# Kernel tuning notes

Measured on AMD Instinct MI355X. Metric: run time of the kernel, lower is better.

The kernel has to match this reference:

```python
import jax, jax.numpy as jnp
import numpy as np

HIDDEN = 256
NUM_REL = 6
NUM_BASES = 30
N_NODES = 50000
N_EDGES = 800000


def rgcn_gate_layer(x, src, dst, etype, basis, att, root, bias, gate_w, gate_b):
    # Basis-decomposed relation weights: W_r = sum_b att[r,b] * basis[b]
    N = x.shape[0]
    W = jnp.einsum('rb,bio->rio', att, basis)           # [R, d, d]
    # Transform all nodes under every relation (cheaper than per-edge matmul
    # since N*R < E), then gather the per-edge message.
    xw = jnp.einsum('nd,rde->rne', x, W)                # [R, N, d]
    msg = xw[etype, src]                                # [E, d]
    # Scalar sigmoid gate per edge message
    g = jax.nn.sigmoid(msg @ gate_w + gate_b)           # [E, 1]
    gated = g * msg
    # Mean aggregation over incoming edges per destination node
    agg = jax.ops.segment_sum(gated, dst, num_segments=N)
    deg = jax.ops.segment_sum(jnp.ones((src.shape[0], 1), x.dtype), dst,
                              num_segments=N)
    agg = agg / jnp.maximum(deg, 1.0)
    return agg + x @ root + bias


def setup_inputs() -> dict:
    key = jax.random.key(0)
    ks = jax.random.split(key, 16)
    d = HIDDEN
    inp = {
        'x': jax.random.normal(ks[0], (N_NODES, d), jnp.float32),
        'edge_src': jax.random.randint(ks[1], (N_EDGES,), 0, N_NODES, jnp.int32),
        'edge_dst': jax.random.randint(ks[2], (N_EDGES,), 0, N_NODES, jnp.int32),
        'edge_type': jax.random.randint(ks[3], (N_EDGES,), 0, NUM_REL, jnp.int32),
    }
    def glorot(k, shape):
        fan = shape[-2] + shape[-1]
        return jax.random.uniform(k, shape, jnp.float32,
                                  -np.sqrt(6.0 / fan), np.sqrt(6.0 / fan))
    for li, off in ((1, 4), (2, 10)):
        inp[f'basis{li}'] = glorot(ks[off + 0], (NUM_BASES, d, d))
        inp[f'att{li}'] = glorot(ks[off + 1], (NUM_REL, NUM_BASES))
        inp[f'root{li}'] = glorot(ks[off + 2], (d, d))
        inp[f'bias{li}'] = jnp.zeros((d,), jnp.float32)
        inp[f'gate_w{li}'] = glorot(ks[off + 3], (d, 1))
        inp[f'gate_b{li}'] = jnp.zeros((1,), jnp.float32)
    return inp


def reference(x, edge_src, edge_dst, edge_type,
              basis1, att1, root1, bias1, gate_w1, gate_b1,
              basis2, att2, root2, bias2, gate_w2, gate_b2):
    h = jax.nn.relu(rgcn_gate_layer(x, edge_src, edge_dst, edge_type,
                                    basis1, att1, root1, bias1,
                                    gate_w1, gate_b1))
    out = rgcn_gate_layer(h, edge_src, edge_dst, edge_type,
                          basis2, att2, root2, bias2, gate_w2, gate_b2)
    return out
```

## Files before the change

kernel.cpp:

```cpp
#include <hip/hip_runtime.h>
#include <cmath>

#define HIDDEN 256
#define NUM_REL 6
#define KA 1536
#define KB 1792
#define NKSTEP 28
#define KASTEP 24
#define CTSTRIDE 28672

typedef float f32x4_t __attribute__((ext_vector_type(4)));
typedef short bf16x8_t __attribute__((ext_vector_type(8)));

__device__ __forceinline__ float bf2f(ushort u) {
  return __uint_as_float(((uint)u) << 16);
}
__device__ __forceinline__ ushort f2bf(float f) {
  uint u = __float_as_uint(f);
  u += 0x7FFFu + ((u >> 16) & 1u);
  return (ushort)(u >> 16);
}

__global__ void compute_W_kernel(const float* __restrict__ att,
                                 const float* __restrict__ basis,
                                 float* __restrict__ Wall) {
  int idx = blockIdx.x * blockDim.x + threadIdx.x;
  int r  = idx >> 16;
  int io = idx & 65535;
  float s = 0.f;
#pragma unroll
  for (int b = 0; b < 30; ++b)
    s += att[r * 30 + b] * basis[(size_t)b * 65536 + io];
  Wall[idx] = s;
}

__global__ __launch_bounds__(256) void gatevec_kernel(
    const float* __restrict__ Wall, const float* __restrict__ gw,
    float* __restrict__ gatevec) {
  const int wave = (blockIdx.x * blockDim.x + threadIdx.x) >> 6;
  const int l = threadIdx.x & 63;
  const int r = wave >> 8, d = wave & 255;
  float4 wv = ((const float4*)(Wall + (size_t)r * 65536 + d * 256))[l];
  float4 gv = ((const float4*)gw)[l];
  float dot = wv.x * gv.x + wv.y * gv.y + wv.z * gv.z + wv.w * gv.w;
#pragma unroll
  for (int off = 32; off; off >>= 1) dot += __shfl_xor(dot, off);
  if (l == 0) gatevec[r * 256 + d] = dot;
}

__global__ void build_BTf(const float* __restrict__ Wall,
                          const float* __restrict__ root,
                          ushort* __restrict__ BTf) {
  int tid = blockIdx.x * blockDim.x + threadIdx.x;
  if (tid >= KB * 256) return;
  int o = tid & 255, gk = tid >> 8;
  int r = gk >> 8, kin = gk & 255;
  float v = (r < 6) ? Wall[(size_t)r * 65536 + kin * 256 + o]
                    : root[(size_t)kin * 256 + o];
  size_t idx = (size_t)(o >> 4) * CTSTRIDE + (size_t)(gk >> 3) * 128 +
               (o & 15) * 8 + (gk & 7);
  BTf[idx] = f2bf(v);
}

__global__ void cvt_f32_bf16(const float* __restrict__ in,
                             ushort* __restrict__ out, int n4) {
  int i = blockIdx.x * blockDim.x + threadIdx.x;
  if (i >= n4) return;
  float4 v = ((const float4*)in)[i];
  ushort4 o;
  o.x = f2bf(v.x); o.y = f2bf(v.y); o.z = f2bf(v.z); o.w = f2bf(v.w);
  ((ushort4*)out)[i] = o;
}

__global__ __launch_bounds__(256) void gdot_kernel(
    const ushort* __restrict__ xb, const float* __restrict__ gatevec,
    const float* __restrict__ gate_b, float* __restrict__ G, int N) {
  const int wave = (blockIdx.x * blockDim.x + threadIdx.x) >> 6;
  if (wave >= N) return;
  const int l = threadIdx.x & 63;
  ushort4 xv = ((const ushort4*)(xb + (size_t)wave * 256))[l];
  const float x0 = bf2f(xv.x), x1 = bf2f(xv.y), x2 = bf2f(xv.z), x3 = bf2f(xv.w);
  float out = 0.f;
#pragma unroll
  for (int r = 0; r < NUM_REL; ++r) {
    float4 gv = ((const float4*)(gatevec + r * 256))[l];
    float d = x0 * gv.x + x1 * gv.y + x2 * gv.z + x3 * gv.w;
#pragma unroll
    for (int off = 32; off; off >>= 1) d += __shfl_xor(d, off);
    if (l == r) out = d;
  }
  if (l < NUM_REL) {
    const float gb = gate_b[0];
    G[(size_t)l * N + wave] = 1.f / (1.f + __expf(-(out + gb)));
  }
}

#define ACCUM(rj, gj, vj)                                                  \
  do {                                                                    \
    const float fx = (gj)*bf2f((vj).x), fy = (gj)*bf2f((vj).y);           \
    const float fz = (gj)*bf2f((vj).z), fw = (gj)*bf2f((vj).w);           \
    switch (rj) {                                                         \
      case 0: a0x += fx; a0y += fy; a0z += fz; a0w += fw; break;          \
      case 1: a1x += fx; a1y += fy; a1z += fz; a1w += fw; break;          \
      case 2: a2x += fx; a2y += fy; a2z += fz; a2w += fw; break;          \
      case 3: a3x += fx; a3y += fy; a3z += fz; a3w += fw; break;          \
      case 4: a4x += fx; a4y += fy; a4z += fz; a4w += fw; break;          \
      default: a5x += fx; a5y += fy; a5z += fz; a5w += fw; break;         \
    }                                                                     \
  } while (0)

#define RELOF(ei) ((ei >= b1) + (ei >= b2) + (ei >= b3) + (ei >= b4) + (ei >= b5))

__global__ __launch_bounds__(256) void edge_agg(
    const ushort* __restrict__ xb, const float* __restrict__ G,
    const int* __restrict__ rp8, const int* __restrict__ src_s,
    ushort* __restrict__ A, int N) {
  const int n = (blockIdx.x * blockDim.x + threadIdx.x) >> 6;
  if (n >= N) return;
  const int l = threadIdx.x & 63;
  const int b0 = rp8[n * 8 + 0], b1 = rp8[n * 8 + 1], b2 = rp8[n * 8 + 2];
  const int b3 = rp8[n * 8 + 3], b4 = rp8[n * 8 + 4], b5 = rp8[n * 8 + 5];
  const int b6 = rp8[n * 8 + 6];

  float a0x = 0, a0y = 0, a0z = 0, a0w = 0, a1x = 0, a1y = 0, a1z = 0, a1w = 0;
  float a2x = 0, a2y = 0, a2z = 0, a2w = 0, a3x = 0, a3y = 0, a3z = 0, a3w = 0;
  float a4x = 0, a4y = 0, a4z = 0, a4w = 0, a5x = 0, a5y = 0, a5z = 0, a5w = 0;

  int e = b0;
  for (; e + 7 < b6; e += 8) {
    const int s0 = src_s[e + 0], s1 = src_s[e + 1];
    const int s2 = src_s[e + 2], s3 = src_s[e + 3];
    const int s4 = src_s[e + 4], s5 = src_s[e + 5];
    const int s6 = src_s[e + 6], s7 = src_s[e + 7];
    const ushort4 v0 = ((const ushort4*)(xb + (size_t)s0 * 256))[l];
    const ushort4 v1 = ((const ushort4*)(xb + (size_t)s1 * 256))[l];
    const ushort4 v2 = ((const ushort4*)(xb + (size_t)s2 * 256))[l];
    const ushort4 v3 = ((const ushort4*)(xb + (size_t)s3 * 256))[l];
    const ushort4 v4 = ((const ushort4*)(xb + (size_t)s4 * 256))[l];
    const ushort4 v5 = ((const ushort4*)(xb + (size_t)s5 * 256))[l];
    const ushort4 v6 = ((const ushort4*)(xb + (size_t)s6 * 256))[l];
    const ushort4 v7 = ((const ushort4*)(xb + (size_t)s7 * 256))[l];
    const int r0 = RELOF(e + 0), r1 = RELOF(e + 1), r2 = RELOF(e + 2),
              r3 = RELOF(e + 3), r4 = RELOF(e + 4), r5 = RELOF(e + 5),
              r6 = RELOF(e + 6), r7 = RELOF(e + 7);
    const float g0 = G[(size_t)r0 * N + s0], g1 = G[(size_t)r1 * N + s1];
    const float g2 = G[(size_t)r2 * N + s2], g3 = G[(size_t)r3 * N + s3];
    const float g4 = G[(size_t)r4 * N + s4], g5 = G[(size_t)r5 * N + s5];
    const float g6 = G[(size_t)r6 * N + s6], g7 = G[(size_t)r7 * N + s7];
    ACCUM(r0, g0, v0); ACCUM(r1, g1, v1); ACCUM(r2, g2, v2); ACCUM(r3, g3, v3);
    ACCUM(r4, g4, v4); ACCUM(r5, g5, v5); ACCUM(r6, g6, v6); ACCUM(r7, g7, v7);
  }
  for (; e < b6; ++e) {
    const int s0 = src_s[e];
    const ushort4 v0 = ((const ushort4*)(xb + (size_t)s0 * 256))[l];
    const int r0 = RELOF(e);
    const float g0 = G[(size_t)r0 * N + s0];
    ACCUM(r0, g0, v0);
  }

  const float inv = 1.f / fmaxf((float)(b6 - b0), 1.f);
  ushort* Arow = A + (size_t)n * KA;
  ushort4 o;
  o.x = f2bf(a0x * inv); o.y = f2bf(a0y * inv); o.z = f2bf(a0z * inv); o.w = f2bf(a0w * inv);
  ((ushort4*)(Arow + 0 * 256))[l] = o;
  o.x = f2bf(a1x * inv); o.y = f2bf(a1y * inv); o.z = f2bf(a1z * inv); o.w = f2bf(a1w * inv);
  ((ushort4*)(Arow + 1 * 256))[l] = o;
  o.x = f2bf(a2x * inv); o.y = f2bf(a2y * inv); o.z = f2bf(a2z * inv); o.w = f2bf(a2w * inv);
  ((ushort4*)(Arow + 2 * 256))[l] = o;
  o.x = f2bf(a3x * inv); o.y = f2bf(a3y * inv); o.z = f2bf(a3z * inv); o.w = f2bf(a3w * inv);
  ((ushort4*)(Arow + 3 * 256))[l] = o;
  o.x = f2bf(a4x * inv); o.y = f2bf(a4y * inv); o.z = f2bf(a4z * inv); o.w = f2bf(a4w * inv);
  ((ushort4*)(Arow + 4 * 256))[l] = o;
  o.x = f2bf(a5x * inv); o.y = f2bf(a5y * inv); o.z = f2bf(a5z * inv); o.w = f2bf(a5w * inv);
  ((ushort4*)(Arow + 5 * 256))[l] = o;
}

__global__ __launch_bounds__(256) void gemm_fused(const ushort* __restrict__ A,
                                                  const ushort* __restrict__ xb,
                                                  const ushort* __restrict__ BTf,
                                                  const float* __restrict__ bias,
                                                  void* __restrict__ outPtr,
                                                  int M, int mode) {
  __shared__ ushort As[3 * 8192];
  const int mB = (M + 127) >> 7;
  const int bid = blockIdx.x;
  const int yb = (bid >> 4) * 8 + (bid & 7);
  if (yb >= mB) return;
  const int colh = (bid >> 3) & 1;
  const int row0 = yb * 128;

  const int tid = threadIdx.x;
  const int w = tid >> 6, l = tid & 63;
  const int wm = w & 1, wn = w >> 1;

  const int srow = l >> 3;
  const int schunk = (l & 7) ^ srow;

  const ushort* Bbase = BTf + (size_t)(colh * 8 + wn * 4) * CTSTRIDE +
                        (l >> 4) * 128 + (l & 15) * 8;

  f32x4_t acc[4][4] = {};

  auto stage = [&](int k, int buf) {
    const int ko = k * 64;
#pragma unroll
    for (int i = 0; i < 4; ++i) {
      const int br = (w * 4 + i) * 8;
      const int ga = min(row0 + br + srow, M - 1);
      const ushort* gp = (k < KASTEP)
          ? (A + (size_t)ga * KA + ko + schunk * 8)
          : (xb + (size_t)ga * 256 + (ko - KA) + schunk * 8);
      __builtin_amdgcn_global_load_lds(
          (const __attribute__((address_space(1))) void*)gp,
          (__attribute__((address_space(3))) void*)(As + buf * 8192 + br * 64),
          16, 0, 0);
    }
  };

  bf16x8_t bc[2][4], bn[2][4];

  stage(0, 0);
  stage(1, 1);
#pragma unroll
  for (int kk = 0; kk < 2; ++kk)
#pragma unroll
    for (int n = 0; n < 4; ++n)
      bc[kk][n] = *(const bf16x8_t*)(Bbase + (size_t)n * CTSTRIDE + kk * 512);

#pragma unroll 2
  for (int k = 0; k < NKSTEP; ++k) {
    const int cur = k % 3;
    asm volatile("s_waitcnt vmcnt(12)" ::: "memory");
    __builtin_amdgcn_s_barrier();
#pragma unroll
    for (int kk = 0; kk < 2; ++kk)
#pragma unroll
      for (int n = 0; n < 4; ++n)
        bn[kk][n] = *(const bf16x8_t*)(Bbase + (size_t)n * CTSTRIDE +
                                       (size_t)(k + 1) * 1024 + kk * 512);
    __builtin_amdgcn_sched_barrier(0);
    if (k + 2 < NKSTEP) stage(k + 2, (k + 2) % 3);

#pragma unroll
    for (int kk = 0; kk < 2; ++kk) {
      const int swc = (kk * 4 + (l >> 4)) ^ (l & 7);
      bf16x8_t a[4];
#pragma unroll
      for (int m = 0; m < 4; ++m) {
        const int rr = wm * 64 + m * 16 + (l & 15);
        a[m] = *(const bf16x8_t*)(As + cur * 8192 + rr * 64 + swc * 8);
      }
#pragma unroll
      for (int m = 0; m < 4; ++m)
#pragma unroll
        for (int n = 0; n < 4; ++n)
          acc[m][n] = __builtin_amdgcn_mfma_f32_16x16x32_bf16(
              a[m], bc[kk][n], acc[m][n], 0, 0, 0);
    }
#pragma unroll
    for (int kk = 0; kk < 2; ++kk)
#pragma unroll
      for (int n = 0; n < 4; ++n)
        bc[kk][n] = bn[kk][n];
  }

  const int rbase = row0 + wm * 64 + (l >> 4) * 4;
  const int cbase = colh * 128 + wn * 64 + (l & 15);
#pragma unroll
  for (int n = 0; n < 4; ++n) {
    const int col = cbase + n * 16;
    const float bv = bias[col];
#pragma unroll
    for (int m = 0; m < 4; ++m)
#pragma unroll
      for (int i = 0; i < 4; ++i) {
        const int row = rbase + m * 16 + i;
        if (row < M) {
          float v = acc[m][n][i] + bv;
          if (mode == 0) {
            v = fmaxf(v, 0.f);
            ((ushort*)outPtr)[(size_t)row * 256 + col] = f2bf(v);
          } else {
            ((float*)outPtr)[(size_t)row * 256 + col] = v;
          }
        }
      }
  }
}

__global__ void hist_kernel(const int* __restrict__ dst,
                            const int* __restrict__ ety,
                            int* __restrict__ cnt, int E) {
  int stride = gridDim.x * blockDim.x;
  for (int e = blockIdx.x * blockDim.x + threadIdx.x; e < E; e += stride)
    atomicAdd(&cnt[dst[e] * 8 + ety[e]], 1);
}

__global__ void scan_reduce(const int* __restrict__ cnt,
                            int* __restrict__ blockSums, int n) {
  __shared__ int sd[256];
  int base = blockIdx.x * 1024;
  int t = threadIdx.x;
  int s = 0;
#pragma unroll
  for (int i = 0; i < 4; ++i) {
    int idx = base + t * 4 + i;
    s += (idx < n) ? cnt[idx] : 0;
  }
  sd[t] = s; __syncthreads();
  for (int off = 128; off; off >>= 1) {
    if (t < off) sd[t] += sd[t + off];
    __syncthreads();
  }
  if (t == 0) blockSums[blockIdx.x] = sd[0];
}

__global__ void scan_offsets(int* __restrict__ blockSums, int nb) {
  __shared__ int sd[512];
  const int t = threadIdx.x;
  const int v = (t < nb) ? blockSums[t] : 0;
  sd[t] = v; __syncthreads();
  for (int off = 1; off < 512; off <<= 1) {
    int u = (t >= off) ? sd[t - off] : 0;
    __syncthreads();
    sd[t] += u;
    __syncthreads();
  }
  if (t < nb) blockSums[t] = sd[t] - v;
}

__global__ void scan_write(const int* __restrict__ cnt,
                           const int* __restrict__ blockSums,
                           int* __restrict__ row_ptr, int n) {
  __shared__ int sd[256];
  int base = blockIdx.x * 1024;
  int t = threadIdx.x;
  int v[4]; int s = 0;
#pragma unroll
  for (int i = 0; i < 4; ++i) {
    int idx = base + t * 4 + i;
    v[i] = (idx < n) ? cnt[idx] : 0;
    s += v[i];
  }
  sd[t] = s; __syncthreads();
  for (int off = 1; off < 256; off <<= 1) {
    int val = (t >= off) ? sd[t - off] : 0;
    __syncthreads();
    sd[t] += val;
    __syncthreads();
  }
  int excl = blockSums[blockIdx.x] + sd[t] - s;
  for (int i = 0; i < 4; ++i) {
    int idx = base + t * 4 + i;
    if (idx < n) {
      row_ptr[idx] = excl;
      excl += v[i];
      if (idx == n - 1) row_ptr[n] = excl;
    }
  }
}

__global__ void scatter_kernel(const int* __restrict__ src,
                               const int* __restrict__ dst,
                               const int* __restrict__ ety,
                               int* __restrict__ cursor,
                               int* __restrict__ src_s, int E) {
  int stride = gridDim.x * blockDim.x;
  for (int e = blockIdx.x * blockDim.x + threadIdx.x; e < E; e += stride) {
    int bin = dst[e] * 8 + ety[e];
    int pos = atomicAdd(&cursor[bin], 1);
    src_s[pos] = src[e];
  }
}

static inline size_t align16(size_t x) { return (x + 15) & ~(size_t)15; }

extern "C" void kernel_launch(void* const* d_in, const int* in_sizes, int n_in,
                              void* d_out, int out_size, void* d_ws,
                              size_t ws_size, hipStream_t stream) {
  const float* x    = (const float*)d_in[0];
  const int*   src  = (const int*)d_in[1];
  const int*   dst  = (const int*)d_in[2];
  const int*   ety  = (const int*)d_in[3];

  const int N   = in_sizes[0] / HIDDEN;
  const int E   = in_sizes[1];
  const int RN2 = N * 8;

  char* p = (char*)d_ws;
  float* Wall    = (float*)p;  p += align16((size_t)NUM_REL * 65536 * 4);
  ushort* BTf    = (ushort*)p; p += align16(((size_t)16 * CTSTRIDE + 1024) * 2);
  float* gatevec = (float*)p;  p += align16((size_t)NUM_REL * 256 * 4);
  float* G       = (float*)p;  p += align16((size_t)NUM_REL * N * 4);
  ushort* xb0    = (ushort*)p; p += align16((size_t)N * HIDDEN * 2);
  ushort* xb1    = (ushort*)p; p += align16((size_t)N * HIDDEN * 2);
  int* cnt       = (int*)p;    p += align16((size_t)RN2 * 4);
  int* cursor    = (int*)p;    p += align16((size_t)RN2 * 4);
  int* row_ptr   = (int*)p;    p += align16((size_t)(RN2 + 1) * 4);
  int* blockSums = (int*)p;    p += 2048;
  int* src_s     = (int*)p;    p += align16((size_t)E * 4);
  ushort* A      = (ushort*)p;

  const int scanBlocks = (RN2 + 1023) / 1024;

  hipMemsetAsync(cnt, 0, (size_t)RN2 * sizeof(int), stream);
  hist_kernel<<<2048, 256, 0, stream>>>(dst, ety, cnt, E);
  scan_reduce<<<scanBlocks, 256, 0, stream>>>(cnt, blockSums, RN2);
  scan_offsets<<<1, 512, 0, stream>>>(blockSums, scanBlocks);
  scan_write<<<scanBlocks, 256, 0, stream>>>(cnt, blockSums, row_ptr, RN2);
  hipMemcpyAsync(cursor, row_ptr, (size_t)RN2 * sizeof(int),
                 hipMemcpyDeviceToDevice, stream);
  scatter_kernel<<<2048, 256, 0, stream>>>(src, dst, ety, cursor, src_s, E);

  cvt_f32_bf16<<<(N * 64 + 255) / 256, 256, 0, stream>>>(x, xb0, N * 64);

  const int nodeBlocks = (N * 64 + 255) / 256;
  const int mBlocks = (N + 127) / 128;
  const int gemmGrid = ((mBlocks + 7) / 8) * 16;

  for (int layer = 0; layer < 2; ++layer) {
    const float* bas  = (const float*)d_in[layer ? 10 : 4];
    const float* att  = (const float*)d_in[layer ? 11 : 5];
    const float* root = (const float*)d_in[layer ? 12 : 6];
    const float* bias = (const float*)d_in[layer ? 13 : 7];
    const float* gw   = (const float*)d_in[layer ? 14 : 8];
    const float* gb   = (const float*)d_in[layer ? 15 : 9];
    const ushort* xb  = layer ? xb1 : xb0;
    void* outp = layer ? d_out : (void*)xb1;
    const int mode = layer ? 1 : 0;

    compute_W_kernel<<<NUM_REL * 65536 / 256, 256, 0, stream>>>(att, bas, Wall);
    gatevec_kernel<<<384, 256, 0, stream>>>(Wall, gw, gatevec);
    build_BTf<<<(KB * 256 + 255) / 256, 256, 0, stream>>>(Wall, root, BTf);
    gdot_kernel<<<nodeBlocks, 256, 0, stream>>>(xb, gatevec, gb, G, N);
    edge_agg<<<nodeBlocks, 256, 0, stream>>>(xb, G, row_ptr, src_s, A, N);
    gemm_fused<<<gemmGrid, 256, 0, stream>>>(A, xb, BTf, bias, outp, N, mode);
  }
}
```

Measured before the change: 542.8 us.

## Fuse weight prep kernels, fold bf16 convert into gdot, retile GEMM to 64x256

Merges compute_W, gatevec and build_BTf into one prep_weights kernel that never materialises the fp32 W buffer. Folds the initial fp32-to-bf16 conversion of x into gdot_kernel and writes the cursor copy inside scan_write, removing a memcpy and a kernel launch. The GEMM changes from 128x128 tiles with 64-wide K steps to 64-row tiles spanning all 256 output columns with 32-wide K steps. Each block now reads its A rows once instead of twice, but it does half the MFMA work per K step and synchronises more often.

```diff
diff --git a/kernel.cpp b/kernel.cpp
--- a/kernel.cpp
+++ b/kernel.cpp
@@ -5,8 +5,8 @@
 #define NUM_REL 6
 #define KA 1536
 #define KB 1792
-#define NKSTEP 28
-#define KASTEP 24
+#define NK 56
+#define NKA 48
 #define CTSTRIDE 28672
 
 typedef float f32x4_t __attribute__((ext_vector_type(4)));
@@ -21,65 +21,53 @@
   return (ushort)(u >> 16);
 }
 
-__global__ void compute_W_kernel(const float* __restrict__ att,
-                                 const float* __restrict__ basis,
-                                 float* __restrict__ Wall) {
-  int idx = blockIdx.x * blockDim.x + threadIdx.x;
-  int r  = idx >> 16;
-  int io = idx & 65535;
-  float s = 0.f;
-#pragma unroll
-  for (int b = 0; b < 30; ++b)
-    s += att[r * 30 + b] * basis[(size_t)b * 65536 + io];
-  Wall[idx] = s;
-}
-
-__global__ __launch_bounds__(256) void gatevec_kernel(
-    const float* __restrict__ Wall, const float* __restrict__ gw,
-    float* __restrict__ gatevec) {
-  const int wave = (blockIdx.x * blockDim.x + threadIdx.x) >> 6;
-  const int l = threadIdx.x & 63;
-  const int r = wave >> 8, d = wave & 255;
-  float4 wv = ((const float4*)(Wall + (size_t)r * 65536 + d * 256))[l];
-  float4 gv = ((const float4*)gw)[l];
-  float dot = wv.x * gv.x + wv.y * gv.y + wv.z * gv.z + wv.w * gv.w;
-#pragma unroll
-  for (int off = 32; off; off >>= 1) dot += __shfl_xor(dot, off);
-  if (l == 0) gatevec[r * 256 + d] = dot;
-}
-
-__global__ void build_BTf(const float* __restrict__ Wall,
-                          const float* __restrict__ root,
-                          ushort* __restrict__ BTf) {
-  int tid = blockIdx.x * blockDim.x + threadIdx.x;
-  if (tid >= KB * 256) return;
-  int o = tid & 255, gk = tid >> 8;
-  int r = gk >> 8, kin = gk & 255;
-  float v = (r < 6) ? Wall[(size_t)r * 65536 + kin * 256 + o]
-                    : root[(size_t)kin * 256 + o];
-  size_t idx = (size_t)(o >> 4) * CTSTRIDE + (size_t)(gk >> 3) * 128 +
-               (o & 15) * 8 + (gk & 7);
-  BTf[idx] = f2bf(v);
-}
-
-__global__ void cvt_f32_bf16(const float* __restrict__ in,
-                             ushort* __restrict__ out, int n4) {
-  int i = blockIdx.x * blockDim.x + threadIdx.x;
-  if (i >= n4) return;
-  float4 v = ((const float4*)in)[i];
-  ushort4 o;
-  o.x = f2bf(v.x); o.y = f2bf(v.y); o.z = f2bf(v.z); o.w = f2bf(v.w);
-  ((ushort4*)out)[i] = o;
+__global__ __launch_bounds__(256) void prep_weights(
+    const float* __restrict__ att, const float* __restrict__ basis,
+    const float* __restrict__ root, const float* __restrict__ gw,
+    ushort* __restrict__ BTf, float* __restrict__ gatevec) {
+  const int d = blockIdx.x, r = blockIdx.y, o = threadIdx.x;
+  float v;
+  if (r < 6) {
+    float s = 0.f;
+#pragma unroll
+    for (int b = 0; b < 30; ++b)
+      s += att[r * 30 + b] * basis[(size_t)b * 65536 + d * 256 + o];
+    v = s;
+  } else {
+    v = root[d * 256 + o];
+  }
+  const int gk = r * 256 + d;
+  BTf[(size_t)(o >> 4) * CTSTRIDE + (gk >> 3) * 128 + (o & 15) * 8 +
+      (gk & 7)] = f2bf(v);
+  if (r < 6) {
+    float t = v * gw[o];
+#pragma unroll
+    for (int off = 32; off; off >>= 1) t += __shfl_xor(t, off);
+    __shared__ float sums[4];
+    if ((o & 63) == 0) sums[o >> 6] = t;
+    __syncthreads();
+    if (o == 0) gatevec[r * 256 + d] = sums[0] + sums[1] + sums[2] + sums[3];
+  }
 }
 
 __global__ __launch_bounds__(256) void gdot_kernel(
-    const ushort* __restrict__ xb, const float* __restrict__ gatevec,
-    const float* __restrict__ gate_b, float* __restrict__ G, int N) {
+    const void* __restrict__ xin, int xIsF32, ushort* __restrict__ xbOut,
+    const float* __restrict__ gatevec, const float* __restrict__ gate_b,
+    float* __restrict__ G, int N) {
   const int wave = (blockIdx.x * blockDim.x + threadIdx.x) >> 6;
   if (wave >= N) return;
   const int l = threadIdx.x & 63;
-  ushort4 xv = ((const ushort4*)(xb + (size_t)wave * 256))[l];
-  const float x0 = bf2f(xv.x), x1 = bf2f(xv.y), x2 = bf2f(xv.z), x3 = bf2f(xv.w);
+  float x0, x1, x2, x3;
+  if (xIsF32) {
+    float4 xv = ((const float4*)xin)[(size_t)wave * 64 + l];
+    x0 = xv.x; x1 = xv.y; x2 = xv.z; x3 = xv.w;
+    ushort4 o;
+    o.x = f2bf(x0); o.y = f2bf(x1); o.z = f2bf(x2); o.w = f2bf(x3);
+    ((ushort4*)xbOut)[(size_t)wave * 64 + l] = o;
+  } else {
+    ushort4 xv = ((const ushort4*)xin)[(size_t)wave * 64 + l];
+    x0 = bf2f(xv.x); x1 = bf2f(xv.y); x2 = bf2f(xv.z); x3 = bf2f(xv.w);
+  }
   float out = 0.f;
 #pragma unroll
   for (int r = 0; r < NUM_REL; ++r) {
@@ -175,97 +163,77 @@
   ((ushort4*)(Arow + 5 * 256))[l] = o;
 }
 
-__global__ __launch_bounds__(256) void gemm_fused(const ushort* __restrict__ A,
-                                                  const ushort* __restrict__ xb,
-                                                  const ushort* __restrict__ BTf,
-                                                  const float* __restrict__ bias,
-                                                  void* __restrict__ outPtr,
-                                                  int M, int mode) {
-  __shared__ ushort As[3 * 8192];
-  const int mB = (M + 127) >> 7;
-  const int bid = blockIdx.x;
-  const int yb = (bid >> 4) * 8 + (bid & 7);
-  if (yb >= mB) return;
-  const int colh = (bid >> 3) & 1;
-  const int row0 = yb * 128;
-
+__global__ __launch_bounds__(256) void gemm_fused(
+    const ushort* __restrict__ A, const ushort* __restrict__ xb,
+    const ushort* __restrict__ BTf, const float* __restrict__ bias,
+    void* __restrict__ outPtr, int M, int mode) {
+  __shared__ ushort As[3][64 * 32];
+  const int row0 = blockIdx.x * 64;
   const int tid = threadIdx.x;
   const int w = tid >> 6, l = tid & 63;
-  const int wm = w & 1, wn = w >> 1;
-
-  const int srow = l >> 3;
-  const int schunk = (l & 7) ^ srow;
-
-  const ushort* Bbase = BTf + (size_t)(colh * 8 + wn * 4) * CTSTRIDE +
-                        (l >> 4) * 128 + (l & 15) * 8;
+
+  const int srow = tid >> 2;
+  const int ssc = (tid & 3) ^ (srow & 3);
+  const int ga = min(row0 + srow, M - 1);
+  const ushort* gpA = A + (size_t)ga * KA + ssc * 8;
+  const ushort* gpX = xb + (size_t)ga * 256 + ssc * 8;
+
+  const ushort* Bb =
+      BTf + (size_t)(w * 4) * CTSTRIDE + (l >> 4) * 128 + (l & 15) * 8;
 
   f32x4_t acc[4][4] = {};
 
   auto stage = [&](int k, int buf) {
-    const int ko = k * 64;
-#pragma unroll
-    for (int i = 0; i < 4; ++i) {
-      const int br = (w * 4 + i) * 8;
-      const int ga = min(row0 + br + srow, M - 1);
-      const ushort* gp = (k < KASTEP)
-          ? (A + (size_t)ga * KA + ko + schunk * 8)
-          : (xb + (size_t)ga * 256 + (ko - KA) + schunk * 8);
-      __builtin_amdgcn_global_load_lds(
-          (const __attribute__((address_space(1))) void*)gp,
-          (__attribute__((address_space(3))) void*)(As + buf * 8192 + br * 64),
-          16, 0, 0);
+    const ushort* gp = (k < NKA) ? (gpA + k * 32) : (gpX + (k * 32 - KA));
+    __builtin_amdgcn_global_load_lds(
+        (const __attribute__((address_space(1))) void*)gp,
+        (__attribute__((address_space(3))) void*)(&As[buf][tid * 8]), 16, 0, 0);
+  };
+
+  auto compute = [&](int buf, const bf16x8_t* b) {
+    bf16x8_t a[4];
+#pragma unroll
+    for (int m = 0; m < 4; ++m) {
+      const int rr = m * 16 + (l & 15);
+      a[m] = *(const bf16x8_t*)(&As[buf][rr * 32 + (((l >> 4) ^ (rr & 3)) * 8)]);
     }
+#pragma unroll
+    for (int m = 0; m < 4; ++m)
+#pragma unroll
+      for (int n = 0; n < 4; ++n)
+        acc[m][n] = __builtin_amdgcn_mfma_f32_16x16x32_bf16(a[m], b[n],
+                                                            acc[m][n], 0, 0, 0);
   };
 
-  bf16x8_t bc[2][4], bn[2][4];
-
+  bf16x8_t bE[4], bO[4];
   stage(0, 0);
   stage(1, 1);
 #pragma unroll
-  for (int kk = 0; kk < 2; ++kk)
+  for (int n = 0; n < 4; ++n)
+    bE[n] = *(const bf16x8_t*)(Bb + (size_t)n * CTSTRIDE);
+
+  for (int k = 0; k < NK; k += 2) {
+    asm volatile("s_waitcnt vmcnt(5)" ::: "memory");
+    __builtin_amdgcn_s_barrier();
 #pragma unroll
     for (int n = 0; n < 4; ++n)
-      bc[kk][n] = *(const bf16x8_t*)(Bbase + (size_t)n * CTSTRIDE + kk * 512);
-
-#pragma unroll 2
-  for (int k = 0; k < NKSTEP; ++k) {
-    const int cur = k % 3;
-    asm volatile("s_waitcnt vmcnt(12)" ::: "memory");
+      bO[n] = *(const bf16x8_t*)(Bb + (size_t)n * CTSTRIDE + (k + 1) * 512);
+    if (k + 2 < NK) stage(k + 2, (k + 2) % 3);
+    compute(k % 3, bE);
+
+    asm volatile("s_waitcnt vmcnt(5)" ::: "memory");
     __builtin_amdgcn_s_barrier();
-#pragma unroll
-    for (int kk = 0; kk < 2; ++kk)
+    if (k + 2 < NK) {
 #pragma unroll
       for (int n = 0; n < 4; ++n)
-        bn[kk][n] = *(const bf16x8_t*)(Bbase + (size_t)n * CTSTRIDE +
-                                       (size_t)(k + 1) * 1024 + kk * 512);
-    __builtin_amdgcn_sched_barrier(0);
-    if (k + 2 < NKSTEP) stage(k + 2, (k + 2) % 3);
-
-#pragma unroll
-    for (int kk = 0; kk < 2; ++kk) {
-      const int swc = (kk * 4 + (l >> 4)) ^ (l & 7);
-      bf16x8_t a[4];
-#pragma unroll
-      for (int m = 0; m < 4; ++m) {
-        const int rr = wm * 64 + m * 16 + (l & 15);
-        a[m] = *(const bf16x8_t*)(As + cur * 8192 + rr * 64 + swc * 8);
-      }
-#pragma unroll
-      for (int m = 0; m < 4; ++m)
-#pragma unroll
-        for (int n = 0; n < 4; ++n)
-          acc[m][n] = __builtin_amdgcn_mfma_f32_16x16x32_bf16(
-              a[m], bc[kk][n], acc[m][n], 0, 0, 0);
+        bE[n] = *(const bf16x8_t*)(Bb + (size_t)n * CTSTRIDE + (k + 2) * 512);
     }
-#pragma unroll
-    for (int kk = 0; kk < 2; ++kk)
-#pragma unroll
-      for (int n = 0; n < 4; ++n)
-        bc[kk][n] = bn[kk][n];
-  }
-
-  const int rbase = row0 + wm * 64 + (l >> 4) * 4;
-  const int cbase = colh * 128 + wn * 64 + (l & 15);
+    if (k + 3 < NK) stage(k + 3, (k + 3) % 3);
+    compute((k + 1) % 3, bO);
+  }
+
+  const int rbase = row0 + (l >> 4) * 4;
+  const int cbase = w * 64 + (l & 15);
 #pragma unroll
   for (int n = 0; n < 4; ++n) {
     const int col = cbase + n * 16;
@@ -331,7 +299,8 @@
 
 __global__ void scan_write(const int* __restrict__ cnt,
                            const int* __restrict__ blockSums,
-                           int* __restrict__ row_ptr, int n) {
+                           int* __restrict__ row_ptr, int* __restrict__ cursor,
+                           int n) {
   __shared__ int sd[256];
   int base = blockIdx.x * 1024;
   int t = threadIdx.x;
@@ -354,6 +323,7 @@
     int idx = base + t * 4 + i;
     if (idx < n) {
       row_ptr[idx] = excl;
+      cursor[idx] = excl;
       excl += v[i];
       if (idx == n - 1) row_ptr[n] = excl;
     }
@@ -388,8 +358,7 @@
   const int RN2 = N * 8;
 
   char* p = (char*)d_ws;
-  float* Wall    = (float*)p;  p += align16((size_t)NUM_REL * 65536 * 4);
-  ushort* BTf    = (ushort*)p; p += align16(((size_t)16 * CTSTRIDE + 1024) * 2);
+  ushort* BTf    = (ushort*)p; p += align16(((size_t)16 * CTSTRIDE + 4096) * 2);
   float* gatevec = (float*)p;  p += align16((size_t)NUM_REL * 256 * 4);
   float* G       = (float*)p;  p += align16((size_t)NUM_REL * N * 4);
   ushort* xb0    = (ushort*)p; p += align16((size_t)N * HIDDEN * 2);
@@ -407,16 +376,12 @@
   hist_kernel<<<2048, 256, 0, stream>>>(dst, ety, cnt, E);
   scan_reduce<<<scanBlocks, 256, 0, stream>>>(cnt, blockSums, RN2);
   scan_offsets<<<1, 512, 0, stream>>>(blockSums, scanBlocks);
-  scan_write<<<scanBlocks, 256, 0, stream>>>(cnt, blockSums, row_ptr, RN2);
-  hipMemcpyAsync(cursor, row_ptr, (size_t)RN2 * sizeof(int),
-                 hipMemcpyDeviceToDevice, stream);
+  scan_write<<<scanBlocks, 256, 0, stream>>>(cnt, blockSums, row_ptr, cursor,
+                                             RN2);
   scatter_kernel<<<2048, 256, 0, stream>>>(src, dst, ety, cursor, src_s, E);
 
-  cvt_f32_bf16<<<(N * 64 + 255) / 256, 256, 0, stream>>>(x, xb0, N * 64);
-
   const int nodeBlocks = (N * 64 + 255) / 256;
-  const int mBlocks = (N + 127) / 128;
-  const int gemmGrid = ((mBlocks + 7) / 8) * 16;
+  const int gemmGrid = (N + 63) / 64;
 
   for (int layer = 0; layer < 2; ++layer) {
     const float* bas  = (const float*)d_in[layer ? 10 : 4];
@@ -429,10 +394,11 @@
     void* outp = layer ? d_out : (void*)xb1;
     const int mode = layer ? 1 : 0;
 
-    compute_W_kernel<<<NUM_REL * 65536 / 256, 256, 0, stream>>>(att, bas, Wall);
-    gatevec_kernel<<<384, 256, 0, stream>>>(Wall, gw, gatevec);
-    build_BTf<<<(KB * 256 + 255) / 256, 256, 0, stream>>>(Wall, root, BTf);
-    gdot_kernel<<<nodeBlocks, 256, 0, stream>>>(xb, gatevec, gb, G, N);
+    prep_weights<<<dim3(256, 7), 256, 0, stream>>>(att, bas, root, gw, BTf,
+                                                   gatevec);
+    gdot_kernel<<<nodeBlocks, 256, 0, stream>>>(
+        layer ? (const void*)xb1 : (const void*)x, layer ? 0 : 1, xb0,
+        gatevec, gb, G, N);
     edge_agg<<<nodeBlocks, 256, 0, stream>>>(xb, G, row_ptr, src_s, A, N);
     gemm_fused<<<gemmGrid, 256, 0, stream>>>(A, xb, BTf, bias, outp, N, mode);
   }
```

After: 512.6 us. 1.06x faster.
